# Kernel tuning notes

Measured on AMD Instinct MI355X. Metric: run time of the kernel, lower is better.

## Reference

```python
import jax, jax.numpy as jnp
import numpy as np

GN_EPS = 1e-5
G = 8          # SKA groups
SKS3 = 27      # sks**3


def _aff(x, s, b):
    # folded BatchNorm (eval): per-channel scale + shift on NCDHW tensor
    return x * s[None, :, None, None, None] + b[None, :, None, None, None]


def _c1(x, w):
    # 1x1x1 conv as channel GEMM; w: [O, I]
    return jnp.einsum('bcdhw,oc->bodhw', x, w)


def _dw5(x, w):
    # depthwise 5x5x5 conv, pad=2; w: [C, 1, 5, 5, 5]
    return jax.lax.conv_general_dilated(
        x, w, window_strides=(1, 1, 1), padding=[(2, 2)] * 3,
        dimension_numbers=('NCDHW', 'OIDHW', 'NCDHW'),
        feature_group_count=x.shape[1])


def setup_inputs() -> dict:
    key = jax.random.key(0)
    ks = jax.random.split(key, 24)
    B, C, D, H, W = 2, 64, 32, 32, 32

    def n(k, shape, scale=1.0):
        return jax.random.normal(k, shape, jnp.float32) * scale

    def u(k, shape):
        return jax.random.uniform(k, shape, jnp.float32, 0.5, 1.5)

    return {
        'x': n(ks[0], (B, C, D, H, W)),
        'w1': n(ks[1], (32, 64), 64 ** -0.5),
        's1': u(ks[2], (32,)), 'b1': n(ks[3], (32,), 0.1),
        'w2': n(ks[4], (32, 1, 5, 5, 5), 125 ** -0.5),
        's2': u(ks[5], (32,)), 'b2': n(ks[6], (32,), 0.1),
        'w3': n(ks[7], (32, 32), 32 ** -0.5),
        's3': u(ks[8], (32,)), 'b3': n(ks[9], (32,), 0.1),
        'w4': n(ks[10], (216, 32), 32 ** -0.5), 'b4': n(ks[11], (216,), 0.1),
        'gn_g': u(ks[12], (216,)), 'gn_b': n(ks[13], (216,), 0.1),
        'bn_s': u(ks[14], (64,)), 'bn_b': n(ks[15], (64,), 0.1),
        'pw1_w': n(ks[16], (128, 64), 64 ** -0.5),
        'pw1_s': u(ks[17], (128,)), 'pw1_b': n(ks[18], (128,), 0.1),
        'pw2_w': n(ks[19], (64, 128), 128 ** -0.5),
        'pw2_s': u(ks[20], (64,)), 'pw2_b': n(ks[21], (64,), 0.1),
    }


def reference(x, w1, s1, b1, w2, s2, b2, w3, s3, b3, w4, b4,
              gn_g, gn_b, bn_s, bn_b,
              pw1_w, pw1_s, pw1_b, pw2_w, pw2_s, pw2_b):
    B, C, D, H, W = x.shape

    # ---- LKP3D: dynamic kernel generation ----
    a = jax.nn.relu(_aff(_c1(x, w1), s1, b1))          # cv1 + BN + ReLU
    a = _aff(_dw5(a, w2), s2, b2)                      # cv2 (5^3 dw) + BN
    a = jax.nn.relu(_aff(_c1(a, w3), s3, b3))          # cv3 + BN + ReLU
    wk = _c1(a, w4) + b4[None, :, None, None, None]    # cv4: [B,216,D,H,W]
    # GroupNorm: num_groups = dim//groups = 8, channels = 216
    g = wk.reshape(B, G, SKS3, D, H, W)
    mu = g.mean(axis=(2, 3, 4, 5), keepdims=True)
    var = g.var(axis=(2, 3, 4, 5), keepdims=True)
    g = (g - mu) * jax.lax.rsqrt(var + GN_EPS)
    wk = g.reshape(B, G * SKS3, D, H, W) * gn_g[None, :, None, None, None] \
         + gn_b[None, :, None, None, None]
    wk = wk.reshape(B, G, SKS3, D, H, W)               # [B, G, 27, D, H, W]

    # ---- SKA3D: apply dynamic kernels (27 shifted copies, grouped) ----
    offs = [(di, hi, wi) for di in (-1, 0, 1) for hi in (-1, 0, 1) for wi in (-1, 0, 1)]
    patches = jnp.stack(
        [jnp.roll(x, (-di, -hi, -wi), axis=(2, 3, 4)) for di, hi, wi in offs],
        axis=2)                                        # [B, C, 27, D, H, W]
    p = patches.reshape(B, G, C // G, SKS3, D, H, W)
    sk = jnp.einsum('bgckdhw,bgkdhw->bgcdhw', p, wk).reshape(B, C, D, H, W)

    y = _aff(sk, bn_s, bn_b) + x                       # LSConv BN + residual

    # ---- FFN (residual): pw1 + BN + ReLU + pw2 + BN ----
    f = jax.nn.relu(_aff(_c1(y, pw1_w), pw1_s, pw1_b))
    f = _aff(_c1(f, pw2_w), pw2_s, pw2_b)
    return y + f
```

## Files before the change

### kernel.cpp

```cpp
#include <hip/hip_runtime.h>
#include <hip/hip_bf16.h>

#define SPAT 32768
#define BATCH 2
#define GN_EPS 1e-5f

__device__ __forceinline__ void fma4(float4& a, const float4& v, float w) {
    a.x = fmaf(v.x, w, a.x); a.y = fmaf(v.y, w, a.y);
    a.z = fmaf(v.z, w, a.z); a.w = fmaf(v.w, w, a.w);
}

template <bool RELU, bool AFF>
__global__ __launch_bounds__(256) void k_c1(
    const float* __restrict__ in, const float* __restrict__ w,
    const float* __restrict__ sc, const float* __restrict__ bi,
    float* __restrict__ out, int Cin, int Cout)
{
    int q = blockIdx.x * 256 + threadIdx.x;
    int s = q * 4;
    int o0 = blockIdx.y * 4, b = blockIdx.z;
    const float* ip = in + (size_t)b * Cin * SPAT + s;
    float4 a0 = {0,0,0,0}, a1 = a0, a2 = a0, a3 = a0;
#pragma unroll 4
    for (int c = 0; c < Cin; ++c) {
        float4 v = *(const float4*)(ip + (size_t)c * SPAT);
        fma4(a0, v, w[(o0+0)*Cin + c]);
        fma4(a1, v, w[(o0+1)*Cin + c]);
        fma4(a2, v, w[(o0+2)*Cin + c]);
        fma4(a3, v, w[(o0+3)*Cin + c]);
    }
    float4 accs[4] = {a0, a1, a2, a3};
#pragma unroll
    for (int i = 0; i < 4; ++i) {
        int o = o0 + i;
        float scale = AFF ? sc[o] : 1.f;
        float shift = bi[o];
        float4 r = accs[i];
        r.x = r.x * scale + shift; r.y = r.y * scale + shift;
        r.z = r.z * scale + shift; r.w = r.w * scale + shift;
        if (RELU) {
            r.x = fmaxf(r.x, 0.f); r.y = fmaxf(r.y, 0.f);
            r.z = fmaxf(r.z, 0.f); r.w = fmaxf(r.w, 0.f);
        }
        *(float4*)(out + ((size_t)b * Cout + o) * SPAT + s) = r;
    }
}

__global__ __launch_bounds__(256) void k_cv4(
    const float* __restrict__ in, const float* __restrict__ w,
    const float* __restrict__ bi, float* __restrict__ out,
    float* __restrict__ partial)
{
    int q = blockIdx.x * 256 + threadIdx.x;
    int s = q * 4;
    int o0 = blockIdx.y * 4, b = blockIdx.z;
    const float* ip = in + (size_t)b * 32 * SPAT + s;
    float4 a0 = {0,0,0,0}, a1 = a0, a2 = a0, a3 = a0;
#pragma unroll 4
    for (int c = 0; c < 32; ++c) {
        float4 v = *(const float4*)(ip + (size_t)c * SPAT);
        fma4(a0, v, w[(o0+0)*32 + c]);
        fma4(a1, v, w[(o0+1)*32 + c]);
        fma4(a2, v, w[(o0+2)*32 + c]);
        fma4(a3, v, w[(o0+3)*32 + c]);
    }
    float4 accs[4] = {a0, a1, a2, a3};
    float sums[4], sss[4];
#pragma unroll
    for (int i = 0; i < 4; ++i) {
        int o = o0 + i;
        float shift = bi[o];
        float4 r = accs[i];
        r.x += shift; r.y += shift; r.z += shift; r.w += shift;
        *(float4*)(out + ((size_t)b * 216 + o) * SPAT + s) = r;
        sums[i] = r.x + r.y + r.z + r.w;
        sss[i]  = r.x*r.x + r.y*r.y + r.z*r.z + r.w*r.w;
    }
#pragma unroll
    for (int off = 32; off > 0; off >>= 1) {
#pragma unroll
        for (int i = 0; i < 4; ++i) {
            sums[i] += __shfl_down(sums[i], off, 64);
            sss[i]  += __shfl_down(sss[i],  off, 64);
        }
    }
    __shared__ float sh[4][4][2];
    int wave = threadIdx.x >> 6, lane = threadIdx.x & 63;
    if (lane == 0) {
#pragma unroll
        for (int i = 0; i < 4; ++i) {
            sh[wave][i][0] = sums[i];
            sh[wave][i][1] = sss[i];
        }
    }
    __syncthreads();
    if (threadIdx.x < 4) {
        int i = threadIdx.x;
        float s0 = sh[0][i][0] + sh[1][i][0] + sh[2][i][0] + sh[3][i][0];
        float s1 = sh[0][i][1] + sh[1][i][1] + sh[2][i][1] + sh[3][i][1];
        int o = o0 + i;
        int idx = (((b * 216 + o) * 32) + blockIdx.x) * 2;
        partial[idx + 0] = s0;
        partial[idx + 1] = s1;
    }
}

__global__ __launch_bounds__(256) void k_gn_stats2(
    const float* __restrict__ partial, float* __restrict__ stats)
{
    int bg = blockIdx.x;
    int b = bg >> 3, g = bg & 7;
    float sum = 0.f, ss = 0.f;
    for (int i = threadIdx.x; i < 27 * 32; i += 256) {
        int o = g * 27 + (i >> 5);
        int xb = i & 31;
        int idx = ((b * 216 + o) * 32 + xb) * 2;
        sum += partial[idx + 0];
        ss  += partial[idx + 1];
    }
    __shared__ float sh[512];
    sh[threadIdx.x] = sum; sh[256 + threadIdx.x] = ss;
    __syncthreads();
    for (int off = 128; off > 0; off >>= 1) {
        if (threadIdx.x < off) {
            sh[threadIdx.x] += sh[threadIdx.x + off];
            sh[256 + threadIdx.x] += sh[256 + threadIdx.x + off];
        }
        __syncthreads();
    }
    if (threadIdx.x == 0) {
        stats[bg * 2 + 0] = sh[0];
        stats[bg * 2 + 1] = sh[256];
    }
}

__global__ __launch_bounds__(256) void k_ska(
    const float* __restrict__ x, const float* __restrict__ wk,
    const float* __restrict__ stats,
    const float* __restrict__ gn_g, const float* __restrict__ gn_b,
    const float* __restrict__ bn_s, const float* __restrict__ bn_b,
    float* __restrict__ y)
{
    int q = blockIdx.x * 256 + threadIdx.x;
    int s = q * 4;
    int g = blockIdx.y, b = blockIdx.z;
    int bg = b * 8 + g;
    const float N = 27.f * (float)SPAT;
    float mu  = stats[bg * 2 + 0] / N;
    float var = stats[bg * 2 + 1] / N - mu * mu;
    float inv = rsqrtf(var + GN_EPS);
    int d = s >> 10, h = (s >> 5) & 31, w0 = s & 31;
    int lane = threadIdx.x & 63;
    int xl_src = (lane & 56) | ((lane + 7) & 7);
    int xr_src = (lane & 56) | ((lane + 1) & 7);
    const float* xg = x + ((size_t)(b * 64 + g * 8)) * SPAT;
    const float* wp = wk + ((size_t)(b * 216 + g * 27)) * SPAT + s;

    float4 acc[8];
    float4 xc[8];
#pragma unroll
    for (int c = 0; c < 8; ++c) acc[c] = {0,0,0,0};

#pragma unroll
    for (int kd = 0; kd < 3; ++kd) {
        int zd = (d + kd + 31) & 31;
#pragma unroll
        for (int kh = 0; kh < 3; ++kh) {
            int zh = (h + kh + 31) & 31;
            int kbase = (kd * 3 + kh) * 3;
            float wn[3][4];
#pragma unroll
            for (int kw = 0; kw < 3; ++kw) {
                int kk = kbase + kw;
                float4 wq = *(const float4*)(wp + (size_t)kk * SPAT);
                float gg = gn_g[g * 27 + kk], gb = gn_b[g * 27 + kk];
                wn[kw][0] = (wq.x - mu) * inv * gg + gb;
                wn[kw][1] = (wq.y - mu) * inv * gg + gb;
                wn[kw][2] = (wq.z - mu) * inv * gg + gb;
                wn[kw][3] = (wq.w - mu) * inv * gg + gb;
            }
            int rowoff = zd * 1024 + zh * 32;
            bool center = (kd == 1) && (kh == 1);
#pragma unroll
            for (int c = 0; c < 8; ++c) {
                float4 m = *(const float4*)(xg + (size_t)c * SPAT + rowoff + w0);
                if (center) xc[c] = m;
                float xl = __shfl(m.w, xl_src, 64);
                float xr = __shfl(m.x, xr_src, 64);
                float win[6] = {xl, m.x, m.y, m.z, m.w, xr};
#pragma unroll
                for (int kw = 0; kw < 3; ++kw) {
                    acc[c].x = fmaf(win[0 + kw], wn[kw][0], acc[c].x);
                    acc[c].y = fmaf(win[1 + kw], wn[kw][1], acc[c].y);
                    acc[c].z = fmaf(win[2 + kw], wn[kw][2], acc[c].z);
                    acc[c].w = fmaf(win[3 + kw], wn[kw][3], acc[c].w);
                }
            }
        }
    }
#pragma unroll
    for (int c = 0; c < 8; ++c) {
        int ch = g * 8 + c;
        float bs = bn_s[ch], bb = bn_b[ch];
        float4 r;
        r.x = acc[c].x * bs + bb + xc[c].x;
        r.y = acc[c].y * bs + bb + xc[c].y;
        r.z = acc[c].z * bs + bb + xc[c].z;
        r.w = acc[c].w * bs + bb + xc[c].w;
        *(float4*)(y + ((size_t)(b * 64 + ch)) * SPAT + s) = r;
    }
}

__global__ __launch_bounds__(256) void k_dw5(
    const float* __restrict__ in, const float* __restrict__ w2,
    const float* __restrict__ s2, const float* __restrict__ b2,
    float* __restrict__ out)
{
    __shared__ float lds[8 * 36 * 40];
    int tid = threadIdx.x;
    int d0 = blockIdx.x * 4;
    int c = blockIdx.y, b = blockIdx.z;
    const float* ip = in + ((size_t)(b * 32 + c)) * SPAT;

    float4 z = {0,0,0,0};
    for (int i = tid; i < 8 * 36 * 40 / 4; i += 256)
        ((float4*)lds)[i] = z;
    __syncthreads();
    for (int i = tid; i < 8 * 256; i += 256) {
        int p = i >> 8, rem = i & 255;
        int r = rem >> 3, c4 = (rem & 7) * 4;
        int d = d0 - 2 + p;
        if (d >= 0 && d < 32) {
            float4 v = *(const float4*)(ip + d * 1024 + r * 32 + c4);
            *(float4*)&lds[p * 1440 + (r + 2) * 40 + (c4 + 4)] = v;
        }
    }
    __syncthreads();

    float scl = s2[c], shf = b2[c];
    const float* wt = w2 + c * 125;
#pragma unroll
    for (int k = 0; k < 4; ++k) {
        int j = tid + k * 256;
        int pd = j >> 8, rem = j & 255;
        int hr = rem >> 3, w4 = (rem & 7) * 4;
        float4 acc = {0,0,0,0};
#pragma unroll
        for (int kd = 0; kd < 5; ++kd) {
            const float* pl = &lds[(pd + kd) * 1440];
#pragma unroll
            for (int kh = 0; kh < 5; ++kh) {
                const float* row = pl + (hr + kh) * 40 + w4;
                float4 r0 = *(const float4*)(row);
                float4 r1 = *(const float4*)(row + 4);
                float4 r2 = *(const float4*)(row + 8);
                float win[12] = {r0.x, r0.y, r0.z, r0.w,
                                 r1.x, r1.y, r1.z, r1.w,
                                 r2.x, r2.y, r2.z, r2.w};
#pragma unroll
                for (int kw = 0; kw < 5; ++kw) {
                    float wv = wt[kd * 25 + kh * 5 + kw];
                    acc.x = fmaf(wv, win[2 + 0 + kw], acc.x);
                    acc.y = fmaf(wv, win[2 + 1 + kw], acc.y);
                    acc.z = fmaf(wv, win[2 + 2 + kw], acc.z);
                    acc.w = fmaf(wv, win[2 + 3 + kw], acc.w);
                }
            }
        }
        acc.x = acc.x * scl + shf; acc.y = acc.y * scl + shf;
        acc.z = acc.z * scl + shf; acc.w = acc.w * scl + shf;
        *(float4*)(out + ((size_t)(b * 32 + c)) * SPAT
                   + (d0 + pd) * 1024 + hr * 32 + w4) = acc;
    }
}

__global__ __launch_bounds__(256) void k_pw2_out(
    const float* __restrict__ f1, const float* __restrict__ w,
    const float* __restrict__ sc, const float* __restrict__ bi,
    const float* __restrict__ yres, float* __restrict__ out)
{
    int q = blockIdx.x * 256 + threadIdx.x;
    int s = q * 4;
    int o0 = blockIdx.y * 4, b = blockIdx.z;
    const float* ip = f1 + (size_t)b * 128 * SPAT + s;
    float4 a0 = {0,0,0,0}, a1 = a0, a2 = a0, a3 = a0;
#pragma unroll 4
    for (int c = 0; c < 128; ++c) {
        float4 v = *(const float4*)(ip + (size_t)c * SPAT);
        fma4(a0, v, w[(o0+0)*128 + c]);
        fma4(a1, v, w[(o0+1)*128 + c]);
        fma4(a2, v, w[(o0+2)*128 + c]);
        fma4(a3, v, w[(o0+3)*128 + c]);
    }
    float4 accs[4] = {a0, a1, a2, a3};
#pragma unroll
    for (int i = 0; i < 4; ++i) {
        int o = o0 + i;
        float scale = sc[o], shift = bi[o];
        float4 yv = *(const float4*)(yres + ((size_t)(b * 64 + o)) * SPAT + s);
        float4 r = accs[i];
        r.x = r.x * scale + shift + yv.x;
        r.y = r.y * scale + shift + yv.y;
        r.z = r.z * scale + shift + yv.z;
        r.w = r.w * scale + shift + yv.w;
        *(float4*)(out + ((size_t)(b * 64 + o)) * SPAT + s) = r;
    }
}

extern "C" void kernel_launch(void* const* d_in, const int* in_sizes, int n_in,
                              void* d_out, int out_size, void* d_ws, size_t ws_size,
                              hipStream_t stream)
{
    const float* x     = (const float*)d_in[0];
    const float* w1    = (const float*)d_in[1];
    const float* s1    = (const float*)d_in[2];
    const float* b1    = (const float*)d_in[3];
    const float* w2    = (const float*)d_in[4];
    const float* s2    = (const float*)d_in[5];
    const float* b2    = (const float*)d_in[6];
    const float* w3    = (const float*)d_in[7];
    const float* s3    = (const float*)d_in[8];
    const float* b3    = (const float*)d_in[9];
    const float* w4    = (const float*)d_in[10];
    const float* b4    = (const float*)d_in[11];
    const float* gn_g  = (const float*)d_in[12];
    const float* gn_b  = (const float*)d_in[13];
    const float* bn_s  = (const float*)d_in[14];
    const float* bn_b  = (const float*)d_in[15];
    const float* pw1_w = (const float*)d_in[16];
    const float* pw1_s = (const float*)d_in[17];
    const float* pw1_b = (const float*)d_in[18];
    const float* pw2_w = (const float*)d_in[19];
    const float* pw2_s = (const float*)d_in[20];
    const float* pw2_b = (const float*)d_in[21];

    float* ws    = (float*)d_ws;
    float* a1    = ws;
    float* a2    = a1 + (size_t)BATCH * 32 * SPAT;
    float* yb    = ws;
    float* wkb   = ws + (size_t)BATCH * 64 * SPAT;
    float* f1    = wkb;
    float* part  = wkb + (size_t)BATCH * 216 * SPAT;
    float* stats = part + BATCH * 216 * 32 * 2;

    dim3 blk(256);
    k_c1<true, true><<<dim3(SPAT / 1024, 8, BATCH), blk, 0, stream>>>(
        x, w1, s1, b1, a1, 64, 32);
    k_dw5<<<dim3(8, 32, BATCH), blk, 0, stream>>>(a1, w2, s2, b2, a2);
    k_c1<true, true><<<dim3(SPAT / 1024, 8, BATCH), blk, 0, stream>>>(
        a2, w3, s3, b3, a1, 32, 32);
    k_cv4<<<dim3(SPAT / 1024, 54, BATCH), blk, 0, stream>>>(
        a1, w4, b4, wkb, part);
    k_gn_stats2<<<dim3(16, 1, 1), blk, 0, stream>>>(part, stats);
    k_ska<<<dim3(SPAT / 1024, 8, BATCH), blk, 0, stream>>>(
        x, wkb, stats, gn_g, gn_b, bn_s, bn_b, yb);
    k_c1<true, true><<<dim3(SPAT / 1024, 32, BATCH), blk, 0, stream>>>(
        yb, pw1_w, pw1_s, pw1_b, f1, 64, 128);
    k_pw2_out<<<dim3(SPAT / 1024, 16, BATCH), blk, 0, stream>>>(
        f1, pw2_w, pw2_s, pw2_b, yb, (float*)d_out);
}
```

Baseline: 231.4 us.

## Widen pointwise conv tiles to 8 outputs and swizzle blocks across XCDs

The pointwise conv kernels (cv1, cv3, cv4, pw1, pw2) now compute 8 output channels per thread instead of 4, halving how many times the input activations are re-read. The grid becomes 1D with a swizzled decode that maps blocks sharing a spatial tile onto the same XCD (bid & 7), so repeated reads of the same input slab can hit that XCD's L2. Input/output channel counts become template constants. More accumulators raise register pressure and halve the block count, which lowers parallelism for the smaller convs.

Measured after the change: 234.3 us. About the same (+1.2%).

```diff
diff --git a/kernel.cpp b/kernel.cpp
--- a/kernel.cpp
+++ b/kernel.cpp
@@ -10,39 +10,51 @@
     a.z = fmaf(v.z, w, a.z); a.w = fmaf(v.w, w, a.w);
 }
 
-template <bool RELU, bool AFF>
-__global__ __launch_bounds__(256) void k_c1(
+template <int OG>
+__device__ __forceinline__ void decode_swz(int bid, int& og, int& b, int& s) {
+    int xcd = bid & 7;
+    int rest = bid >> 3;
+    og = rest % OG;
+    int pair = rest / OG;
+    int spb = pair * 8 + xcd;
+    b = spb >> 5;
+    s = (spb & 31) * 1024 + threadIdx.x * 4;
+}
+
+template <int CIN, int COUT, bool RELU, bool AFF>
+__global__ __launch_bounds__(256) void k_pw(
     const float* __restrict__ in, const float* __restrict__ w,
     const float* __restrict__ sc, const float* __restrict__ bi,
-    float* __restrict__ out, int Cin, int Cout)
-{
-    int q = blockIdx.x * 256 + threadIdx.x;
-    int s = q * 4;
-    int o0 = blockIdx.y * 4, b = blockIdx.z;
-    const float* ip = in + (size_t)b * Cin * SPAT + s;
-    float4 a0 = {0,0,0,0}, a1 = a0, a2 = a0, a3 = a0;
+    float* __restrict__ out)
+{
+    constexpr int OG = COUT / 8;
+    int og, b, s;
+    decode_swz<OG>(blockIdx.x, og, b, s);
+    int o0 = og * 8;
+    const float* ip = in + (size_t)b * CIN * SPAT + s;
+    float4 acc[8];
+#pragma unroll
+    for (int i = 0; i < 8; ++i) acc[i] = {0, 0, 0, 0};
 #pragma unroll 4
-    for (int c = 0; c < Cin; ++c) {
+    for (int c = 0; c < CIN; ++c) {
         float4 v = *(const float4*)(ip + (size_t)c * SPAT);
-        fma4(a0, v, w[(o0+0)*Cin + c]);
-        fma4(a1, v, w[(o0+1)*Cin + c]);
-        fma4(a2, v, w[(o0+2)*Cin + c]);
-        fma4(a3, v, w[(o0+3)*Cin + c]);
-    }
-    float4 accs[4] = {a0, a1, a2, a3};
-#pragma unroll
-    for (int i = 0; i < 4; ++i) {
+#pragma unroll
+        for (int i = 0; i < 8; ++i)
+            fma4(acc[i], v, w[(o0 + i) * CIN + c]);
+    }
+#pragma unroll
+    for (int i = 0; i < 8; ++i) {
         int o = o0 + i;
         float scale = AFF ? sc[o] : 1.f;
         float shift = bi[o];
-        float4 r = accs[i];
+        float4 r = acc[i];
         r.x = r.x * scale + shift; r.y = r.y * scale + shift;
         r.z = r.z * scale + shift; r.w = r.w * scale + shift;
         if (RELU) {
             r.x = fmaxf(r.x, 0.f); r.y = fmaxf(r.y, 0.f);
             r.z = fmaxf(r.z, 0.f); r.w = fmaxf(r.w, 0.f);
         }
-        *(float4*)(out + ((size_t)b * Cout + o) * SPAT + s) = r;
+        *(float4*)(out + ((size_t)b * COUT + o) * SPAT + s) = r;
     }
 }
 
@@ -51,55 +63,56 @@
     const float* __restrict__ bi, float* __restrict__ out,
     float* __restrict__ partial)
 {
-    int q = blockIdx.x * 256 + threadIdx.x;
-    int s = q * 4;
-    int o0 = blockIdx.y * 4, b = blockIdx.z;
+    int og, b, s;
+    decode_swz<27>(blockIdx.x, og, b, s);
+    int sp = s >> 10;
+    int o0 = og * 8;
     const float* ip = in + (size_t)b * 32 * SPAT + s;
-    float4 a0 = {0,0,0,0}, a1 = a0, a2 = a0, a3 = a0;
+    float4 acc[8];
+#pragma unroll
+    for (int i = 0; i < 8; ++i) acc[i] = {0, 0, 0, 0};
 #pragma unroll 4
     for (int c = 0; c < 32; ++c) {
         float4 v = *(const float4*)(ip + (size_t)c * SPAT);
-        fma4(a0, v, w[(o0+0)*32 + c]);
-        fma4(a1, v, w[(o0+1)*32 + c]);
-        fma4(a2, v, w[(o0+2)*32 + c]);
-        fma4(a3, v, w[(o0+3)*32 + c]);
-    }
-    float4 accs[4] = {a0, a1, a2, a3};
-    float sums[4], sss[4];
-#pragma unroll
-    for (int i = 0; i < 4; ++i) {
+#pragma unroll
+        for (int i = 0; i < 8; ++i)
+            fma4(acc[i], v, w[(o0 + i) * 32 + c]);
+    }
+    float sums[8], sss[8];
+#pragma unroll
+    for (int i = 0; i < 8; ++i) {
         int o = o0 + i;
         float shift = bi[o];
-        float4 r = accs[i];
+        float4 r = acc[i];
         r.x += shift; r.y += shift; r.z += shift; r.w += shift;
         *(float4*)(out + ((size_t)b * 216 + o) * SPAT + s) = r;
         sums[i] = r.x + r.y + r.z + r.w;
-        sss[i]  = r.x*r.x + r.y*r.y + r.z*r.z + r.w*r.w;
+        sss[i]  = r.x * r.x + r.y * r.y + r.z * r.z + r.w * r.w;
     }
 #pragma unroll
     for (int off = 32; off > 0; off >>= 1) {
 #pragma unroll
-        for (int i = 0; i < 4; ++i) {
+        for (int i = 0; i < 8; ++i) {
             sums[i] += __shfl_down(sums[i], off, 64);
             sss[i]  += __shfl_down(sss[i],  off, 64);
         }
     }
-    __shared__ float sh[4][4][2];
+    __shared__ float sh[4][8][2];
     int wave = threadIdx.x >> 6, lane = threadIdx.x & 63;
     if (lane == 0) {
 #pragma unroll
-        for (int i = 0; i < 4; ++i) {
+        for (int i = 0; i < 8; ++i) {
             sh[wave][i][0] = sums[i];
             sh[wave][i][1] = sss[i];
         }
     }
     __syncthreads();
-    if (threadIdx.x < 4) {
+    if (threadIdx.x < 8) {
         int i = threadIdx.x;
         float s0 = sh[0][i][0] + sh[1][i][0] + sh[2][i][0] + sh[3][i][0];
         float s1 = sh[0][i][1] + sh[1][i][1] + sh[2][i][1] + sh[3][i][1];
         int o = o0 + i;
-        int idx = (((b * 216 + o) * 32) + blockIdx.x) * 2;
+        int idx = ((b * 216 + o) * 32 + sp) * 2;
         partial[idx + 0] = s0;
         partial[idx + 1] = s1;
     }
@@ -159,7 +172,7 @@
     float4 acc[8];
     float4 xc[8];
 #pragma unroll
-    for (int c = 0; c < 8; ++c) acc[c] = {0,0,0,0};
+    for (int c = 0; c < 8; ++c) acc[c] = {0, 0, 0, 0};
 
 #pragma unroll
     for (int kd = 0; kd < 3; ++kd) {
@@ -222,7 +235,7 @@
     int c = blockIdx.y, b = blockIdx.z;
     const float* ip = in + ((size_t)(b * 32 + c)) * SPAT;
 
-    float4 z = {0,0,0,0};
+    float4 z = {0, 0, 0, 0};
     for (int i = tid; i < 8 * 36 * 40 / 4; i += 256)
         ((float4*)lds)[i] = z;
     __syncthreads();
@@ -244,7 +257,7 @@
         int j = tid + k * 256;
         int pd = j >> 8, rem = j & 255;
         int hr = rem >> 3, w4 = (rem & 7) * 4;
-        float4 acc = {0,0,0,0};
+        float4 acc = {0, 0, 0, 0};
 #pragma unroll
         for (int kd = 0; kd < 5; ++kd) {
             const float* pl = &lds[(pd + kd) * 1440];
@@ -279,26 +292,26 @@
     const float* __restrict__ sc, const float* __restrict__ bi,
     const float* __restrict__ yres, float* __restrict__ out)
 {
-    int q = blockIdx.x * 256 + threadIdx.x;
-    int s = q * 4;
-    int o0 = blockIdx.y * 4, b = blockIdx.z;
+    int og, b, s;
+    decode_swz<8>(blockIdx.x, og, b, s);
+    int o0 = og * 8;
     const float* ip = f1 + (size_t)b * 128 * SPAT + s;
-    float4 a0 = {0,0,0,0}, a1 = a0, a2 = a0, a3 = a0;
+    float4 acc[8];
+#pragma unroll
+    for (int i = 0; i < 8; ++i) acc[i] = {0, 0, 0, 0};
 #pragma unroll 4
     for (int c = 0; c < 128; ++c) {
         float4 v = *(const float4*)(ip + (size_t)c * SPAT);
-        fma4(a0, v, w[(o0+0)*128 + c]);
-        fma4(a1, v, w[(o0+1)*128 + c]);
-        fma4(a2, v, w[(o0+2)*128 + c]);
-        fma4(a3, v, w[(o0+3)*128 + c]);
-    }
-    float4 accs[4] = {a0, a1, a2, a3};
-#pragma unroll
-    for (int i = 0; i < 4; ++i) {
+#pragma unroll
+        for (int i = 0; i < 8; ++i)
+            fma4(acc[i], v, w[(o0 + i) * 128 + c]);
+    }
+#pragma unroll
+    for (int i = 0; i < 8; ++i) {
         int o = o0 + i;
         float scale = sc[o], shift = bi[o];
         float4 yv = *(const float4*)(yres + ((size_t)(b * 64 + o)) * SPAT + s);
-        float4 r = accs[i];
+        float4 r = acc[i];
         r.x = r.x * scale + shift + yv.x;
         r.y = r.y * scale + shift + yv.y;
         r.z = r.z * scale + shift + yv.z;
@@ -344,18 +357,15 @@
     float* stats = part + BATCH * 216 * 32 * 2;
 
     dim3 blk(256);
-    k_c1<true, true><<<dim3(SPAT / 1024, 8, BATCH), blk, 0, stream>>>(
-        x, w1, s1, b1, a1, 64, 32);
+    k_pw<64, 32, true, true><<<dim3(4 * 64), blk, 0, stream>>>(x, w1, s1, b1, a1);
     k_dw5<<<dim3(8, 32, BATCH), blk, 0, stream>>>(a1, w2, s2, b2, a2);
-    k_c1<true, true><<<dim3(SPAT / 1024, 8, BATCH), blk, 0, stream>>>(
-        a2, w3, s3, b3, a1, 32, 32);
-    k_cv4<<<dim3(SPAT / 1024, 54, BATCH), blk, 0, stream>>>(
-        a1, w4, b4, wkb, part);
-    k_gn_stats2<<<dim3(16, 1, 1), blk, 0, stream>>>(part, stats);
+    k_pw<32, 32, true, true><<<dim3(4 * 64), blk, 0, stream>>>(a2, w3, s3, b3, a1);
+    k_cv4<<<dim3(27 * 64), blk, 0, stream>>>(a1, w4, b4, wkb, part);
+    k_gn_stats2<<<dim3(16), blk, 0, stream>>>(part, stats);
     k_ska<<<dim3(SPAT / 1024, 8, BATCH), blk, 0, stream>>>(
         x, wkb, stats, gn_g, gn_b, bn_s, bn_b, yb);
-    k_c1<true, true><<<dim3(SPAT / 1024, 32, BATCH), blk, 0, stream>>>(
-        yb, pw1_w, pw1_s, pw1_b, f1, 64, 128);
-    k_pw2_out<<<dim3(SPAT / 1024, 16, BATCH), blk, 0, stream>>>(
+    k_pw<64, 128, true, true><<<dim3(16 * 64), blk, 0, stream>>>(
+        yb, pw1_w, pw1_s, pw1_b, f1);
+    k_pw2_out<<<dim3(8 * 64), blk, 0, stream>>>(
         f1, pw2_w, pw2_s, pw2_b, yb, (float*)d_out);
 }
```
